# Performance work log

Measured on AMD Instinct MI355X. Metric: run time of the kernel, lower is better.

Reference implementation:

```python
import jax, jax.numpy as jnp
import numpy as np
import math

B, T, C = 32, 256, 1024
LAYER_ID, NUM_LAYERS = 12, 24
NEG_INF = -1e38


def setup_inputs() -> dict:
    key = jax.random.key(0)
    ks = jax.random.split(key, 5)
    x = jax.random.normal(ks[0], (B, T, C), dtype=jnp.float32)
    # deterministic parameter init, faithful to the torch __init__
    r01 = LAYER_ID / (NUM_LAYERS - 1)          # ratio_0_to_1
    r10 = 1.0 - LAYER_ID / NUM_LAYERS          # ratio_1_to_almost0
    h = jnp.arange(C, dtype=jnp.float32)
    time_decay = -5.0 + 8.0 * (h / (C - 1)) ** (0.7 + 1.3 * r01)
    tf = (jnp.arange(C) + 1) % 3 - 1
    time_first = jnp.full((C,), math.log(0.3), jnp.float32) + 0.5 * tf.astype(jnp.float32)
    xr = (jnp.arange(C, dtype=jnp.float32) / C)[None, None, :]   # [1,1,C]
    time_mix_k = xr ** r10
    time_mix_v = xr ** r10 + 0.3 * r01
    time_mix_r = xr ** (0.5 * r10)
    s = 1.0 / math.sqrt(C)
    Wk = jax.random.normal(ks[1], (C, C), jnp.float32) * s
    Wv = jax.random.normal(ks[2], (C, C), jnp.float32) * s
    Wr = jax.random.normal(ks[3], (C, C), jnp.float32) * s
    Wo = jax.random.normal(ks[4], (C, C), jnp.float32) * s
    return {"x": x, "time_decay": time_decay, "time_first": time_first,
            "time_mix_k": time_mix_k, "time_mix_v": time_mix_v, "time_mix_r": time_mix_r,
            "Wk": Wk, "Wv": Wv, "Wr": Wr, "Wo": Wo}


def wkv(time_decay, time_first, k, v):
    """Numerically-stabilized WKV scan. k,v: [B,T,C]; decay/first: [C]."""
    w = -jnp.exp(time_decay)   # per-channel log-decay (negative)
    u = time_first
    kT = jnp.swapaxes(k, 0, 1)  # [T,B,C]
    vT = jnp.swapaxes(v, 0, 1)

    def step(carry, kv):
        p, q, o = carry                       # p,q: running num/den; o: log scale
        kt, vt = kv                           # [B,C]
        no = jnp.maximum(o, u + kt)
        A = jnp.exp(o - no)
        Bc = jnp.exp(u + kt - no)
        y = (A * p + Bc * vt) / (A * q + Bc)
        no2 = jnp.maximum(w + o, kt)
        A2 = jnp.exp(w + o - no2)
        B2 = jnp.exp(kt - no2)
        return (A2 * p + B2 * vt, A2 * q + B2, no2), y

    init = (jnp.zeros((k.shape[0], k.shape[2]), k.dtype),
            jnp.zeros((k.shape[0], k.shape[2]), k.dtype),
            jnp.full((k.shape[0], k.shape[2]), NEG_INF, k.dtype))
    _, yT = jax.lax.scan(step, init, (kT, vT))
    return jnp.swapaxes(yT, 0, 1)  # [B,T,C]


def reference(x, time_decay, time_first, time_mix_k, time_mix_v, time_mix_r, Wk, Wv, Wr, Wo):
    # time_shift: xx[t] = x[t-1], xx[0] = 0
    xx = jnp.pad(x, ((0, 0), (1, 0), (0, 0)))[:, :-1, :]
    xk = x * time_mix_k + xx * (1.0 - time_mix_k)
    xv = x * time_mix_v + xx * (1.0 - time_mix_v)
    xr = x * time_mix_r + xx * (1.0 - time_mix_r)
    k = jnp.einsum('btc,dc->btd', xk, Wk)
    v = jnp.einsum('btc,dc->btd', xv, Wv)
    r = jnp.einsum('btc,dc->btd', xr, Wr)
    sr = jax.nn.sigmoid(r)
    rwkv = sr * wkv(time_decay, time_first, k, v)
    return jnp.einsum('btc,dc->btd', rwkv, Wo)
```

## Files before the change

### kernel.cpp

```cpp
#include <hip/hip_runtime.h>

#define Bdim 32
#define Tdim 256
#define Cdim 1024
#define Mrows (Bdim * Tdim)

typedef unsigned short u16;
typedef unsigned int u32;
typedef __bf16 bf16x8 __attribute__((ext_vector_type(8)));
typedef float f32x4 __attribute__((ext_vector_type(4)));

__device__ __forceinline__ float bf2f(u32 u) {
    union { u32 i; float f; } v; v.i = u << 16; return v.f;
}
__device__ __forceinline__ u16 f2bf(float f) {
    union { float f; u32 i; } v; v.f = f;
    u32 u = v.i;
    return (u16)((u + 0x7fffu + ((u >> 16) & 1u)) >> 16);
}

__device__ __forceinline__ void gload16(const u16* g, u16* l) {
    __builtin_amdgcn_global_load_lds(
        (__attribute__((address_space(1))) const void*)g,
        (__attribute__((address_space(3))) void*)l, 16, 0, 0);
}

__global__ __launch_bounds__(256) void prep_fused(
    const float* __restrict__ x, const float* __restrict__ tmk,
    const float* __restrict__ tmv, const float* __restrict__ tmr,
    u16* __restrict__ xk, u16* __restrict__ xv, u16* __restrict__ xr,
    const float* __restrict__ w0, const float* __restrict__ w1,
    const float* __restrict__ w2, const float* __restrict__ w3,
    u16* __restrict__ o0, u16* __restrict__ o1,
    u16* __restrict__ o2, u16* __restrict__ o3)
{
    int bid = blockIdx.x;
    if (bid < 4096) {
        int tid = bid * 256 + threadIdx.x;
        int e = tid << 3;
        int c = e & (Cdim - 1);
        int t = (e >> 10) & (Tdim - 1);
        float xf[8], xxf[8], mk[8], mv[8], mr[8];
        *(float4*)(xf)     = *(const float4*)(x + e);
        *(float4*)(xf + 4) = *(const float4*)(x + e + 4);
        if (t != 0) {
            *(float4*)(xxf)     = *(const float4*)(x + e - Cdim);
            *(float4*)(xxf + 4) = *(const float4*)(x + e - Cdim + 4);
        } else {
#pragma unroll
            for (int j = 0; j < 8; j++) xxf[j] = 0.f;
        }
        *(float4*)(mk)     = *(const float4*)(tmk + c);
        *(float4*)(mk + 4) = *(const float4*)(tmk + c + 4);
        *(float4*)(mv)     = *(const float4*)(tmv + c);
        *(float4*)(mv + 4) = *(const float4*)(tmv + c + 4);
        *(float4*)(mr)     = *(const float4*)(tmr + c);
        *(float4*)(mr + 4) = *(const float4*)(tmr + c + 4);
        u16 ok[8], ov[8], orr[8];
#pragma unroll
        for (int j = 0; j < 8; j++) {
            float d = xf[j] - xxf[j];
            ok[j]  = f2bf(xxf[j] + d * mk[j]);
            ov[j]  = f2bf(xxf[j] + d * mv[j]);
            orr[j] = f2bf(xxf[j] + d * mr[j]);
        }
        *(uint4*)(xk + e) = *(const uint4*)ok;
        *(uint4*)(xv + e) = *(const uint4*)ov;
        *(uint4*)(xr + e) = *(const uint4*)orr;
    } else {
        int wb = bid - 4096;
        int m = wb >> 9;
        const float* src; u16* dst;
        switch (m) {
            case 0: src = w0; dst = o0; break;
            case 1: src = w1; dst = o1; break;
            case 2: src = w2; dst = o2; break;
            default: src = w3; dst = o3; break;
        }
        int i = (((wb & 511) << 8) + threadIdx.x) << 3;
        float a[8];
        *(float4*)(a)     = *(const float4*)(src + i);
        *(float4*)(a + 4) = *(const float4*)(src + i + 4);
        u16 o[8];
#pragma unroll
        for (int j = 0; j < 8; j++) o[j] = f2bf(a[j]);
        *(uint4*)(dst + i) = *(const uint4*)o;
    }
}

template <int BF16OUT>
__device__ __forceinline__ void gemm_body(
    const u16* __restrict__ A, const u16* __restrict__ Bw, void* __restrict__ Cout,
    u16* As0, u16* Bs0, u16* As1, u16* Bs1, int bm, int bn)
{
    const int K = Cdim, N = Cdim;
    const int tid = threadIdx.x;
    const int lane = tid & 63, wave = tid >> 6;
    const int wm = (wave & 1) << 6, wn = (wave >> 1) << 6;
    const int fr = lane & 15, quad = lane >> 4;

    const int srow = tid >> 2;
    const int skc = ((((tid & 3) + ((tid >> 3) & 3)) & 3) << 3);
    const u16* ga = A + (size_t)(bm * 128 + srow) * K + skc;
    const u16* gb = Bw + (size_t)(bn * 128 + srow) * K + skc;
    u16* la0 = As0 + (wave << 9);
    u16* lb0 = Bs0 + (wave << 9);
    u16* la1 = As1 + (wave << 9);
    u16* lb1 = Bs1 + (wave << 9);
    const size_t gstep = (size_t)64 * K;

    f32x4 acc[4][4];
#pragma unroll
    for (int i = 0; i < 4; i++)
#pragma unroll
        for (int j = 0; j < 4; j++)
            acc[i][j] = (f32x4){0.f, 0.f, 0.f, 0.f};

    const int rq = (((quad - ((fr >> 1) & 3)) & 3) << 3);

    for (int k0 = 0; k0 < K; k0 += 64) {
        __syncthreads();
        gload16(ga, la0);
        gload16(ga + gstep, la0 + 2048);
        gload16(gb, lb0);
        gload16(gb + gstep, lb0 + 2048);
        gload16(ga + 32, la1);
        gload16(ga + 32 + gstep, la1 + 2048);
        gload16(gb + 32, lb1);
        gload16(gb + 32 + gstep, lb1 + 2048);
        ga += 64; gb += 64;
        __syncthreads();
#pragma unroll
        for (int h = 0; h < 2; h++) {
            const u16* Ah = h ? As1 : As0;
            const u16* Bh = h ? Bs1 : Bs0;
            bf16x8 af[4], bfr[4];
#pragma unroll
            for (int i = 0; i < 4; i++) {
                af[i]  = *(const bf16x8*)(Ah + (wm + i * 16 + fr) * 32 + rq);
                bfr[i] = *(const bf16x8*)(Bh + (wn + i * 16 + fr) * 32 + rq);
            }
#pragma unroll
            for (int i = 0; i < 4; i++)
#pragma unroll
                for (int j = 0; j < 4; j++)
                    acc[i][j] = __builtin_amdgcn_mfma_f32_16x16x32_bf16(
                        af[i], bfr[j], acc[i][j], 0, 0, 0);
        }
    }

    const int gr0 = bm * 128 + wm + quad * 4;
    const int gc0 = bn * 128 + wn + fr;
#pragma unroll
    for (int i = 0; i < 4; i++)
#pragma unroll
        for (int j = 0; j < 4; j++)
#pragma unroll
            for (int r = 0; r < 4; r++) {
                int gr = gr0 + i * 16 + r;
                int gc = gc0 + j * 16;
                float val = acc[i][j][r];
                if (BF16OUT)
                    ((u16*)Cout)[(size_t)gr * N + gc] = f2bf(val);
                else
                    ((float*)Cout)[(size_t)gr * N + gc] = val;
            }
}

__global__ __launch_bounds__(256) void gemm3_kernel(
    const u16* __restrict__ xk, const u16* __restrict__ xv, const u16* __restrict__ xr,
    const u16* __restrict__ wk, const u16* __restrict__ wv, const u16* __restrict__ wr,
    u16* __restrict__ ck, u16* __restrict__ cv, u16* __restrict__ cr)
{
    __shared__ u16 As0[128 * 32], Bs0[128 * 32], As1[128 * 32], Bs1[128 * 32];
    const u16* A; const u16* Bw; u16* Cout;
    switch (blockIdx.z) {
        case 0:  A = xk; Bw = wk; Cout = ck; break;
        case 1:  A = xv; Bw = wv; Cout = cv; break;
        default: A = xr; Bw = wr; Cout = cr; break;
    }
    int bx = blockIdx.x;
    gemm_body<1>(A, Bw, (void*)Cout, As0, Bs0, As1, Bs1, bx & 63, bx >> 6);
}

__global__ __launch_bounds__(256) void gemmo_kernel(
    const u16* __restrict__ A, const u16* __restrict__ Bw, float* __restrict__ Cout)
{
    __shared__ u16 As0[128 * 32], Bs0[128 * 32], As1[128 * 32], Bs1[128 * 32];
    int bx = blockIdx.x;
    gemm_body<0>(A, Bw, (void*)Cout, As0, Bs0, As1, Bs1, bx & 63, bx >> 6);
}

#define WTC 16

#define LOADCHUNK(KA, VA, RA, T0)                                        \
    _Pragma("unroll")                                                    \
    for (int s = 0; s < WTC; s++) {                                      \
        size_t idx = base + (size_t)((T0) + s) * Cdim;                   \
        KA[s] = kb[idx]; VA[s] = vb[idx]; RA[s] = rb[idx];               \
    }

#define COMPCHUNK(KA, VA, RA, T0)                                        \
    _Pragma("unroll")                                                    \
    for (int s = 0; s < WTC; s++) {                                      \
        float kt = bf2f(KA[s]);                                          \
        float vt = bf2f(VA[s]);                                          \
        float rt = bf2f(RA[s]);                                          \
        float uk = u + kt;                                               \
        float no = fmaxf(o, uk);                                         \
        float Ae = __expf(o - no);                                       \
        float Bc = __expf(uk - no);                                      \
        float num = Ae * p + Bc * vt;                                    \
        float den = Ae * q + Bc;                                         \
        float y = num * __builtin_amdgcn_rcpf(den);                      \
        float sr = __builtin_amdgcn_rcpf(1.f + __expf(-rt));             \
        rwkv[base + (size_t)((T0) + s) * Cdim] = f2bf(y * sr);           \
        float wo = w + o;                                                \
        float no2 = fmaxf(wo, kt);                                       \
        float A2 = __expf(wo - no2);                                     \
        float B2 = __expf(kt - no2);                                     \
        p = A2 * p + B2 * vt;                                            \
        q = A2 * q + B2;                                                 \
        o = no2;                                                         \
    }

__global__ __launch_bounds__(64) void wkv_kernel(
    const u16* __restrict__ kb, const u16* __restrict__ vb,
    const u16* __restrict__ rb, const float* __restrict__ td,
    const float* __restrict__ tfirst, u16* __restrict__ rwkv)
{
    int lane = threadIdx.x;
    int blk = blockIdx.x;
    int b = blk >> 4;
    int c = ((blk & 15) << 6) + lane;
    float w = -__expf(td[c]);
    float u = tfirst[c];
    const size_t base = (size_t)b * Tdim * Cdim + c;

    u32 kA[WTC], vA[WTC], rA[WTC];
    u32 kB[WTC], vB[WTC], rB[WTC];
    float p = 0.f, q = 0.f, o = -1e38f;

    LOADCHUNK(kA, vA, rA, 0)
    for (int t0 = 0; t0 < Tdim; t0 += 2 * WTC) {
        LOADCHUNK(kB, vB, rB, t0 + WTC)
        COMPCHUNK(kA, vA, rA, t0)
        if (t0 + 2 * WTC < Tdim) {
            LOADCHUNK(kA, vA, rA, t0 + 2 * WTC)
        }
        COMPCHUNK(kB, vB, rB, t0 + WTC)
    }
}

extern "C" void kernel_launch(void* const* d_in, const int* in_sizes, int n_in,
                              void* d_out, int out_size, void* d_ws, size_t ws_size,
                              hipStream_t stream) {
    (void)in_sizes; (void)n_in; (void)out_size; (void)ws_size;
    const float* x   = (const float*)d_in[0];
    const float* td  = (const float*)d_in[1];
    const float* tfi = (const float*)d_in[2];
    const float* tmk = (const float*)d_in[3];
    const float* tmv = (const float*)d_in[4];
    const float* tmr = (const float*)d_in[5];
    const float* Wk  = (const float*)d_in[6];
    const float* Wv  = (const float*)d_in[7];
    const float* Wr  = (const float*)d_in[8];
    const float* Wo  = (const float*)d_in[9];

    char* ws = (char*)d_ws;
    const size_t MiB = (size_t)1 << 20;
    u16* xk    = (u16*)(ws);
    u16* xv    = (u16*)(ws + 16 * MiB);
    u16* xr    = (u16*)(ws + 32 * MiB);
    u16* wkb   = (u16*)(ws + 48 * MiB);
    u16* wvb   = (u16*)(ws + 50 * MiB);
    u16* wrb   = (u16*)(ws + 52 * MiB);
    u16* wob   = (u16*)(ws + 54 * MiB);
    u16* kb    = (u16*)(ws + 56 * MiB);
    u16* vb    = (u16*)(ws + 72 * MiB);
    u16* rb    = (u16*)(ws + 88 * MiB);
    u16* rwkvb = (u16*)(ws);

    prep_fused<<<6144, 256, 0, stream>>>(x, tmk, tmv, tmr, xk, xv, xr,
                                         Wk, Wv, Wr, Wo, wkb, wvb, wrb, wob);

    gemm3_kernel<<<dim3(512, 1, 3), 256, 0, stream>>>(xk, xv, xr, wkb, wvb, wrb,
                                                      kb, vb, rb);

    wkv_kernel<<<512, 64, 0, stream>>>(kb, vb, rb, td, tfi, rwkvb);

    gemmo_kernel<<<512, 256, 0, stream>>>(rwkvb, wob, (float*)d_out);
}
```

Before: 227.4 us.

## Use 256x128 GEMM tiles with 8 waves and triple-buffered async LDS pipeline

```diff
diff --git a/kernel.cpp b/kernel.cpp
--- a/kernel.cpp
+++ b/kernel.cpp
@@ -3,7 +3,6 @@
 #define Bdim 32
 #define Tdim 256
 #define Cdim 1024
-#define Mrows (Bdim * Tdim)
 
 typedef unsigned short u16;
 typedef unsigned int u32;
@@ -89,25 +88,27 @@
 }
 
 template <int BF16OUT>
-__device__ __forceinline__ void gemm_body(
+__device__ __forceinline__ void gemm_body256(
     const u16* __restrict__ A, const u16* __restrict__ Bw, void* __restrict__ Cout,
-    u16* As0, u16* Bs0, u16* As1, u16* Bs1, int bm, int bn)
+    u16* As, u16* Bs, int bm, int bn)
 {
     const int K = Cdim, N = Cdim;
+    const int NT = K / 64;
     const int tid = threadIdx.x;
     const int lane = tid & 63, wave = tid >> 6;
-    const int wm = (wave & 1) << 6, wn = (wave >> 1) << 6;
+    const int wm = (wave >> 1) << 6;
+    const int wn = (wave & 1) << 6;
     const int fr = lane & 15, quad = lane >> 4;
-
-    const int srow = tid >> 2;
-    const int skc = ((((tid & 3) + ((tid >> 3) & 3)) & 3) << 3);
-    const u16* ga = A + (size_t)(bm * 128 + srow) * K + skc;
-    const u16* gb = Bw + (size_t)(bn * 128 + srow) * K + skc;
-    u16* la0 = As0 + (wave << 9);
-    u16* lb0 = Bs0 + (wave << 9);
-    u16* la1 = As1 + (wave << 9);
-    u16* lb1 = Bs1 + (wave << 9);
-    const size_t gstep = (size_t)64 * K;
+    const int lwo = wave << 9;
+
+    const int srow = tid >> 3;
+    const int schunk = ((tid & 7) ^ (srow & 7)) << 3;
+    const u16* gaS = A  + (size_t)(bm * 256 + srow) * K + schunk;
+    const u16* gbS = Bw + (size_t)(bn * 128 + srow) * K + schunk;
+    const size_t rstep = (size_t)64 * K;
+
+    const int koff0 = ((quad << 3))      ^ ((fr & 7) << 3);
+    const int koff1 = (32 + (quad << 3)) ^ ((fr & 7) << 3);
 
     f32x4 acc[4][4];
 #pragma unroll
@@ -116,40 +117,80 @@
         for (int j = 0; j < 4; j++)
             acc[i][j] = (f32x4){0.f, 0.f, 0.f, 0.f};
 
-    const int rq = (((quad - ((fr >> 1) & 3)) & 3) << 3);
-
-    for (int k0 = 0; k0 < K; k0 += 64) {
-        __syncthreads();
-        gload16(ga, la0);
-        gload16(ga + gstep, la0 + 2048);
-        gload16(gb, lb0);
-        gload16(gb + gstep, lb0 + 2048);
-        gload16(ga + 32, la1);
-        gload16(ga + 32 + gstep, la1 + 2048);
-        gload16(gb + 32, lb1);
-        gload16(gb + 32 + gstep, lb1 + 2048);
-        ga += 64; gb += 64;
-        __syncthreads();
-#pragma unroll
-        for (int h = 0; h < 2; h++) {
-            const u16* Ah = h ? As1 : As0;
-            const u16* Bh = h ? Bs1 : Bs0;
-            bf16x8 af[4], bfr[4];
-#pragma unroll
-            for (int i = 0; i < 4; i++) {
-                af[i]  = *(const bf16x8*)(Ah + (wm + i * 16 + fr) * 32 + rq);
-                bfr[i] = *(const bf16x8*)(Bh + (wn + i * 16 + fr) * 32 + rq);
+    auto issue2 = [&](int T, int aoff, int boff) {
+        const u16* ga = gaS + T * 64;
+        u16* la = As + aoff + lwo;
+        gload16(ga,             la);
+        gload16(ga + rstep,     la + 4096);
+        gload16(ga + 2 * rstep, la + 8192);
+        gload16(ga + 3 * rstep, la + 12288);
+        const u16* gb = gbS + T * 64;
+        u16* lb = Bs + boff + lwo;
+        gload16(gb,         lb);
+        gload16(gb + rstep, lb + 4096);
+    };
+
+    auto compute_tile = [&](int ac, int bc) {
+        const u16* __restrict__ Ab = As + ac;
+        const u16* __restrict__ Bb = Bs + bc;
+        __builtin_amdgcn_s_setprio(1);
+#pragma unroll
+        for (int ph = 0; ph < 4; ++ph) {
+            const int qi = ph >> 1, qj = ph & 1;
+            bf16x8 af[2][2], bfr[2][2];
+#pragma unroll
+            for (int d = 0; d < 2; ++d) {
+                const int ra = (wm + (qi * 2 + d) * 16 + fr) << 6;
+                af[d][0] = *(const bf16x8*)(Ab + ra + koff0);
+                af[d][1] = *(const bf16x8*)(Ab + ra + koff1);
+                const int rb = (wn + (qj * 2 + d) * 16 + fr) << 6;
+                bfr[d][0] = *(const bf16x8*)(Bb + rb + koff0);
+                bfr[d][1] = *(const bf16x8*)(Bb + rb + koff1);
             }
 #pragma unroll
-            for (int i = 0; i < 4; i++)
-#pragma unroll
-                for (int j = 0; j < 4; j++)
-                    acc[i][j] = __builtin_amdgcn_mfma_f32_16x16x32_bf16(
-                        af[i], bfr[j], acc[i][j], 0, 0, 0);
-        }
-    }
-
-    const int gr0 = bm * 128 + wm + quad * 4;
+            for (int di = 0; di < 2; ++di)
+#pragma unroll
+                for (int dj = 0; dj < 2; ++dj) {
+                    acc[qi * 2 + di][qj * 2 + dj] =
+                        __builtin_amdgcn_mfma_f32_16x16x32_bf16(
+                            af[di][0], bfr[dj][0], acc[qi * 2 + di][qj * 2 + dj], 0, 0, 0);
+                    acc[qi * 2 + di][qj * 2 + dj] =
+                        __builtin_amdgcn_mfma_f32_16x16x32_bf16(
+                            af[di][1], bfr[dj][1], acc[qi * 2 + di][qj * 2 + dj], 0, 0, 0);
+                }
+        }
+        __builtin_amdgcn_s_setprio(0);
+    };
+
+    issue2(0, 0, 0);
+    issue2(1, 16384, 8192);
+    asm volatile("s_waitcnt vmcnt(6)" ::: "memory");
+    __builtin_amdgcn_s_barrier();
+    __builtin_amdgcn_sched_barrier(0);
+
+    int a_c = 0, b_c = 0;
+    int a_s = 32768, b_s = 16384;
+#pragma unroll 1
+    for (int t = 0; t <= NT - 3; ++t) {
+        issue2(t + 2, a_s, b_s);
+        compute_tile(a_c, b_c);
+        asm volatile("s_waitcnt vmcnt(6)" ::: "memory");
+        __builtin_amdgcn_s_barrier();
+        __builtin_amdgcn_sched_barrier(0);
+        a_c += 16384; if (a_c == 49152) a_c = 0;
+        b_c += 8192;  if (b_c == 24576) b_c = 0;
+        a_s += 16384; if (a_s == 49152) a_s = 0;
+        b_s += 8192;  if (b_s == 24576) b_s = 0;
+    }
+    compute_tile(a_c, b_c);
+    asm volatile("s_waitcnt vmcnt(0)" ::: "memory");
+    __builtin_amdgcn_s_barrier();
+    __builtin_amdgcn_sched_barrier(0);
+    a_c += 16384; if (a_c == 49152) a_c = 0;
+    b_c += 8192;  if (b_c == 24576) b_c = 0;
+    compute_tile(a_c, b_c);
+
+    const int gr0 = bm * 256 + wm + quad * 4;
     const int gc0 = bn * 128 + wn + fr;
 #pragma unroll
     for (int i = 0; i < 4; i++)
@@ -167,12 +208,13 @@
             }
 }
 
-__global__ __launch_bounds__(256) void gemm3_kernel(
+__global__ __launch_bounds__(512) void gemm3_kernel(
     const u16* __restrict__ xk, const u16* __restrict__ xv, const u16* __restrict__ xr,
     const u16* __restrict__ wk, const u16* __restrict__ wv, const u16* __restrict__ wr,
     u16* __restrict__ ck, u16* __restrict__ cv, u16* __restrict__ cr)
 {
-    __shared__ u16 As0[128 * 32], Bs0[128 * 32], As1[128 * 32], Bs1[128 * 32];
+    __shared__ __align__(16) u16 As[3 * 16384];
+    __shared__ __align__(16) u16 Bs[3 * 8192];
     const u16* A; const u16* Bw; u16* Cout;
     switch (blockIdx.z) {
         case 0:  A = xk; Bw = wk; Cout = ck; break;
@@ -180,15 +222,16 @@
         default: A = xr; Bw = wr; Cout = cr; break;
     }
     int bx = blockIdx.x;
-    gemm_body<1>(A, Bw, (void*)Cout, As0, Bs0, As1, Bs1, bx & 63, bx >> 6);
-}
-
-__global__ __launch_bounds__(256) void gemmo_kernel(
+    gemm_body256<1>(A, Bw, (void*)Cout, As, Bs, bx & 31, bx >> 5);
+}
+
+__global__ __launch_bounds__(512) void gemmo_kernel(
     const u16* __restrict__ A, const u16* __restrict__ Bw, float* __restrict__ Cout)
 {
-    __shared__ u16 As0[128 * 32], Bs0[128 * 32], As1[128 * 32], Bs1[128 * 32];
+    __shared__ __align__(16) u16 As[3 * 16384];
+    __shared__ __align__(16) u16 Bs[3 * 8192];
     int bx = blockIdx.x;
-    gemm_body<0>(A, Bw, (void*)Cout, As0, Bs0, As1, Bs1, bx & 63, bx >> 6);
+    gemm_body256<0>(A, Bw, (void*)Cout, As, Bs, bx & 31, bx >> 5);
 }
 
 #define WTC 16
@@ -284,10 +327,10 @@
     prep_fused<<<6144, 256, 0, stream>>>(x, tmk, tmv, tmr, xk, xv, xr,
                                          Wk, Wv, Wr, Wo, wkb, wvb, wrb, wob);
 
-    gemm3_kernel<<<dim3(512, 1, 3), 256, 0, stream>>>(xk, xv, xr, wkb, wvb, wrb,
+    gemm3_kernel<<<dim3(256, 1, 3), 512, 0, stream>>>(xk, xv, xr, wkb, wvb, wrb,
                                                       kb, vb, rb);
 
     wkv_kernel<<<512, 64, 0, stream>>>(kb, vb, rb, td, tfi, rwkvb);
 
-    gemmo_kernel<<<512, 256, 0, stream>>>(rwkvb, wob, (float*)d_out);
-}
+    gemmo_kernel<<<256, 512, 0, stream>>>(rwkvb, wob, (float*)d_out);
+}
```

Result: slower. 243.7 us (+7.2%).

## Rewrite GEMMs with 256x256 tiles and phased double-buffered LDS pipeline

Applied to the files above, without the earlier changes.

```diff
diff --git a/kernel.cpp b/kernel.cpp
--- a/kernel.cpp
+++ b/kernel.cpp
@@ -3,7 +3,6 @@
 #define Bdim 32
 #define Tdim 256
 #define Cdim 1024
-#define Mrows (Bdim * Tdim)
 
 typedef unsigned short u16;
 typedef unsigned int u32;
@@ -89,70 +88,153 @@
 }
 
 template <int BF16OUT>
-__device__ __forceinline__ void gemm_body(
+__device__ __forceinline__ void gemm_body256(
     const u16* __restrict__ A, const u16* __restrict__ Bw, void* __restrict__ Cout,
-    u16* As0, u16* Bs0, u16* As1, u16* Bs1, int bm, int bn)
+    u16* __restrict__ Ls, int bm, int bn)
 {
     const int K = Cdim, N = Cdim;
+    const int NT = K / 64;
     const int tid = threadIdx.x;
     const int lane = tid & 63, wave = tid >> 6;
-    const int wm = (wave & 1) << 6, wn = (wave >> 1) << 6;
+    const int wm = wave >> 2;
+    const int wn = wave & 3;
     const int fr = lane & 15, quad = lane >> 4;
-
-    const int srow = tid >> 2;
-    const int skc = ((((tid & 3) + ((tid >> 3) & 3)) & 3) << 3);
-    const u16* ga = A + (size_t)(bm * 128 + srow) * K + skc;
-    const u16* gb = Bw + (size_t)(bn * 128 + srow) * K + skc;
-    u16* la0 = As0 + (wave << 9);
-    u16* lb0 = Bs0 + (wave << 9);
-    u16* la1 = As1 + (wave << 9);
-    u16* lb1 = Bs1 + (wave << 9);
-    const size_t gstep = (size_t)64 * K;
-
-    f32x4 acc[4][4];
-#pragma unroll
-    for (int i = 0; i < 4; i++)
+    const int fr7 = fr & 7;
+
+    const int srow = tid >> 3;
+    const int schunk = ((tid & 7) ^ (srow & 7)) << 3;
+    const u16* gA = A + (size_t)(bm * 256 + srow) * K + schunk;
+    const int gbrow = ((srow >> 5) << 6) + (srow & 31);
+    const u16* gB = Bw + (size_t)(bn * 256 + gbrow) * K + schunk;
+    u16* lA = Ls + (wave << 9);
+    u16* lB = Ls + 32768 + (wave << 9);
+
+    auto stAX = [&](int T, int buf) {
+        const u16* g = gA + T * 64;
+        u16* l = lA + buf * 16384;
+        gload16(g,                   l);
+        gload16(g + (size_t)128 * K, l + 4096);
+    };
+    auto stBX = [&](int T, int buf) {
+        const u16* g = gB + T * 64;
+        u16* l = lB + buf * 16384;
+        gload16(g,                   l);
+        gload16(g + (size_t)128 * K, l + 4096);
+    };
+    auto stBY = [&](int T, int buf) {
+        const u16* g = gB + T * 64;
+        u16* l = lB + buf * 16384;
+        gload16(g + (size_t)32 * K,  l + 8192);
+        gload16(g + (size_t)160 * K, l + 12288);
+    };
+    auto stAY = [&](int T, int buf) {
+        const u16* g = gA + T * 64;
+        u16* l = lA + buf * 16384;
+        gload16(g + (size_t)64 * K,  l + 8192);
+        gload16(g + (size_t)192 * K, l + 12288);
+    };
+
+    const int arX = wm * 64 + fr;
+    const int brX = wn * 32 + fr;
+
+    f32x4 acc[8][4];
+#pragma unroll
+    for (int i = 0; i < 8; i++)
 #pragma unroll
         for (int j = 0; j < 4; j++)
             acc[i][j] = (f32x4){0.f, 0.f, 0.f, 0.f};
 
-    const int rq = (((quad - ((fr >> 1) & 3)) & 3) << 3);
-
-    for (int k0 = 0; k0 < K; k0 += 64) {
-        __syncthreads();
-        gload16(ga, la0);
-        gload16(ga + gstep, la0 + 2048);
-        gload16(gb, lb0);
-        gload16(gb + gstep, lb0 + 2048);
-        gload16(ga + 32, la1);
-        gload16(ga + 32 + gstep, la1 + 2048);
-        gload16(gb + 32, lb1);
-        gload16(gb + 32 + gstep, lb1 + 2048);
-        ga += 64; gb += 64;
-        __syncthreads();
-#pragma unroll
-        for (int h = 0; h < 2; h++) {
-            const u16* Ah = h ? As1 : As0;
-            const u16* Bh = h ? Bs1 : Bs0;
-            bf16x8 af[4], bfr[4];
-#pragma unroll
-            for (int i = 0; i < 4; i++) {
-                af[i]  = *(const bf16x8*)(Ah + (wm + i * 16 + fr) * 32 + rq);
-                bfr[i] = *(const bf16x8*)(Bh + (wn + i * 16 + fr) * 32 + rq);
-            }
-#pragma unroll
-            for (int i = 0; i < 4; i++)
-#pragma unroll
-                for (int j = 0; j < 4; j++)
-                    acc[i][j] = __builtin_amdgcn_mfma_f32_16x16x32_bf16(
-                        af[i], bfr[j], acc[i][j], 0, 0, 0);
-        }
-    }
-
-    const int gr0 = bm * 128 + wm + quad * 4;
-    const int gc0 = bn * 128 + wn + fr;
-#pragma unroll
-    for (int i = 0; i < 4; i++)
+    bf16x8 af[4][2], b0[2][2], b1[2][2];
+
+#define KOFF(s) ((((s << 2) + quad) ^ fr7) << 3)
+#define MFMA_Q(I0, J0, BFR)                                                   \
+    _Pragma("unroll")                                                         \
+    for (int s = 0; s < 2; ++s)                                               \
+        _Pragma("unroll")                                                     \
+        for (int i = 0; i < 4; ++i)                                           \
+            _Pragma("unroll")                                                 \
+            for (int j = 0; j < 2; ++j)                                       \
+                acc[(I0) + i][(J0) + j] = __builtin_amdgcn_mfma_f32_16x16x32_bf16( \
+                    af[i][s], BFR[j][s], acc[(I0) + i][(J0) + j], 0, 0, 0);
+
+    stAX(0, 0); stBX(0, 0); stBY(0, 0); stAY(0, 0);
+    asm volatile("s_waitcnt vmcnt(4)" ::: "memory");
+    __builtin_amdgcn_s_barrier();
+
+#pragma unroll 1
+    for (int t = 0; t < NT; ++t) {
+        const int buf = t & 1, nb = buf ^ 1;
+        const u16* __restrict__ Ab = Ls + buf * 16384;
+        const u16* __restrict__ Bb = Ls + 32768 + buf * 16384;
+        const bool st = (t + 1 < NT);
+
+#pragma unroll
+        for (int i = 0; i < 4; ++i)
+#pragma unroll
+            for (int s = 0; s < 2; ++s)
+                af[i][s] = *(const bf16x8*)(Ab + (arX + i * 16) * 64 + KOFF(s));
+#pragma unroll
+        for (int j = 0; j < 2; ++j)
+#pragma unroll
+            for (int s = 0; s < 2; ++s)
+                b0[j][s] = *(const bf16x8*)(Bb + (brX + j * 16) * 64 + KOFF(s));
+        if (st) stAX(t + 1, nb);
+        __builtin_amdgcn_s_barrier();
+        asm volatile("s_waitcnt lgkmcnt(0)" ::: "memory");
+        __builtin_amdgcn_sched_barrier(0);
+        __builtin_amdgcn_s_setprio(1);
+        MFMA_Q(0, 0, b0)
+        __builtin_amdgcn_s_setprio(0);
+        if (st) { asm volatile("s_waitcnt vmcnt(4)" ::: "memory"); }
+        else    { asm volatile("s_waitcnt vmcnt(2)" ::: "memory"); }
+        __builtin_amdgcn_s_barrier();
+
+#pragma unroll
+        for (int j = 0; j < 2; ++j)
+#pragma unroll
+            for (int s = 0; s < 2; ++s)
+                b1[j][s] = *(const bf16x8*)(Bb + (128 + brX + j * 16) * 64 + KOFF(s));
+        if (st) stBX(t + 1, nb);
+        __builtin_amdgcn_s_barrier();
+        asm volatile("s_waitcnt lgkmcnt(0)" ::: "memory");
+        __builtin_amdgcn_sched_barrier(0);
+        __builtin_amdgcn_s_setprio(1);
+        MFMA_Q(0, 2, b1)
+        __builtin_amdgcn_s_setprio(0);
+        if (st) { asm volatile("s_waitcnt vmcnt(4)" ::: "memory"); }
+        else    { asm volatile("s_waitcnt vmcnt(0)" ::: "memory"); }
+        __builtin_amdgcn_s_barrier();
+
+#pragma unroll
+        for (int i = 0; i < 4; ++i)
+#pragma unroll
+            for (int s = 0; s < 2; ++s)
+                af[i][s] = *(const bf16x8*)(Ab + (128 + arX + i * 16) * 64 + KOFF(s));
+        if (st) stBY(t + 1, nb);
+        __builtin_amdgcn_s_barrier();
+        asm volatile("s_waitcnt lgkmcnt(0)" ::: "memory");
+        __builtin_amdgcn_sched_barrier(0);
+        __builtin_amdgcn_s_setprio(1);
+        MFMA_Q(4, 2, b1)
+        __builtin_amdgcn_s_setprio(0);
+        if (st) { asm volatile("s_waitcnt vmcnt(4)" ::: "memory"); }
+        __builtin_amdgcn_s_barrier();
+
+        if (st) stAY(t + 1, nb);
+        __builtin_amdgcn_s_barrier();
+        __builtin_amdgcn_s_setprio(1);
+        MFMA_Q(4, 0, b0)
+        __builtin_amdgcn_s_setprio(0);
+        if (st) { asm volatile("s_waitcnt vmcnt(4)" ::: "memory"); }
+        __builtin_amdgcn_s_barrier();
+    }
+#undef MFMA_Q
+#undef KOFF
+
+    const int gr0 = bm * 256 + wm * 128 + quad * 4;
+    const int gc0 = bn * 256 + wn * 64 + fr;
+#pragma unroll
+    for (int i = 0; i < 8; i++)
 #pragma unroll
         for (int j = 0; j < 4; j++)
 #pragma unroll
@@ -167,12 +249,12 @@
             }
 }
 
-__global__ __launch_bounds__(256) void gemm3_kernel(
+__global__ __launch_bounds__(512, 2) void gemm3_kernel(
     const u16* __restrict__ xk, const u16* __restrict__ xv, const u16* __restrict__ xr,
     const u16* __restrict__ wk, const u16* __restrict__ wv, const u16* __restrict__ wr,
     u16* __restrict__ ck, u16* __restrict__ cv, u16* __restrict__ cr)
 {
-    __shared__ u16 As0[128 * 32], Bs0[128 * 32], As1[128 * 32], Bs1[128 * 32];
+    __shared__ __align__(16) u16 Ls[4 * 16384];
     const u16* A; const u16* Bw; u16* Cout;
     switch (blockIdx.z) {
         case 0:  A = xk; Bw = wk; Cout = ck; break;
@@ -180,15 +262,15 @@
         default: A = xr; Bw = wr; Cout = cr; break;
     }
     int bx = blockIdx.x;
-    gemm_body<1>(A, Bw, (void*)Cout, As0, Bs0, As1, Bs1, bx & 63, bx >> 6);
-}
-
-__global__ __launch_bounds__(256) void gemmo_kernel(
+    gemm_body256<1>(A, Bw, (void*)Cout, Ls, bx & 31, bx >> 5);
+}
+
+__global__ __launch_bounds__(512, 2) void gemmo_kernel(
     const u16* __restrict__ A, const u16* __restrict__ Bw, float* __restrict__ Cout)
 {
-    __shared__ u16 As0[128 * 32], Bs0[128 * 32], As1[128 * 32], Bs1[128 * 32];
+    __shared__ __align__(16) u16 Ls[4 * 16384];
     int bx = blockIdx.x;
-    gemm_body<0>(A, Bw, (void*)Cout, As0, Bs0, As1, Bs1, bx & 63, bx >> 6);
+    gemm_body256<0>(A, Bw, (void*)Cout, Ls, bx & 31, bx >> 5);
 }
 
 #define WTC 16
@@ -284,10 +366,10 @@
     prep_fused<<<6144, 256, 0, stream>>>(x, tmk, tmv, tmr, xk, xv, xr,
                                          Wk, Wv, Wr, Wo, wkb, wvb, wrb, wob);
 
-    gemm3_kernel<<<dim3(512, 1, 3), 256, 0, stream>>>(xk, xv, xr, wkb, wvb, wrb,
+    gemm3_kernel<<<dim3(128, 1, 3), 512, 0, stream>>>(xk, xv, xr, wkb, wvb, wrb,
                                                       kb, vb, rb);
 
     wkv_kernel<<<512, 64, 0, stream>>>(kb, vb, rb, td, tfi, rwkvb);
 
-    gemmo_kernel<<<512, 256, 0, stream>>>(rwkvb, wob, (float*)d_out);
-}
+    gemmo_kernel<<<128, 512, 0, stream>>>(rwkvb, wob, (float*)d_out);
+}
```

Result: slower. 240.4 us (+5.7%).

## Double-buffer GEMM LDS tiles to overlap global loads with MFMA compute

Applied to the files above, without the earlier changes.

```diff
diff --git a/kernel.cpp b/kernel.cpp
--- a/kernel.cpp
+++ b/kernel.cpp
@@ -3,7 +3,6 @@
 #define Bdim 32
 #define Tdim 256
 #define Cdim 1024
-#define Mrows (Bdim * Tdim)
 
 typedef unsigned short u16;
 typedef unsigned int u32;
@@ -91,9 +90,10 @@
 template <int BF16OUT>
 __device__ __forceinline__ void gemm_body(
     const u16* __restrict__ A, const u16* __restrict__ Bw, void* __restrict__ Cout,
-    u16* As0, u16* Bs0, u16* As1, u16* Bs1, int bm, int bn)
+    u16* __restrict__ Ls, int bm, int bn)
 {
     const int K = Cdim, N = Cdim;
+    const int NT = K / 64;
     const int tid = threadIdx.x;
     const int lane = tid & 63, wave = tid >> 6;
     const int wm = (wave & 1) << 6, wn = (wave >> 1) << 6;
@@ -103,11 +103,22 @@
     const int skc = ((((tid & 3) + ((tid >> 3) & 3)) & 3) << 3);
     const u16* ga = A + (size_t)(bm * 128 + srow) * K + skc;
     const u16* gb = Bw + (size_t)(bn * 128 + srow) * K + skc;
-    u16* la0 = As0 + (wave << 9);
-    u16* lb0 = Bs0 + (wave << 9);
-    u16* la1 = As1 + (wave << 9);
-    u16* lb1 = Bs1 + (wave << 9);
     const size_t gstep = (size_t)64 * K;
+    const int lw = wave << 9;
+
+    auto stage = [&](int t, int buf) {
+        const u16* gat = ga + t * 64;
+        const u16* gbt = gb + t * 64;
+        u16* base = Ls + buf * 16384 + lw;
+        gload16(gat,              base);
+        gload16(gat + gstep,      base + 2048);
+        gload16(gbt,              base + 4096);
+        gload16(gbt + gstep,      base + 4096 + 2048);
+        gload16(gat + 32,         base + 8192);
+        gload16(gat + 32 + gstep, base + 8192 + 2048);
+        gload16(gbt + 32,         base + 12288);
+        gload16(gbt + 32 + gstep, base + 12288 + 2048);
+    };
 
     f32x4 acc[4][4];
 #pragma unroll
@@ -118,22 +129,19 @@
 
     const int rq = (((quad - ((fr >> 1) & 3)) & 3) << 3);
 
-    for (int k0 = 0; k0 < K; k0 += 64) {
-        __syncthreads();
-        gload16(ga, la0);
-        gload16(ga + gstep, la0 + 2048);
-        gload16(gb, lb0);
-        gload16(gb + gstep, lb0 + 2048);
-        gload16(ga + 32, la1);
-        gload16(ga + 32 + gstep, la1 + 2048);
-        gload16(gb + 32, lb1);
-        gload16(gb + 32 + gstep, lb1 + 2048);
-        ga += 64; gb += 64;
-        __syncthreads();
+    stage(0, 0);
+    asm volatile("s_waitcnt vmcnt(0)" ::: "memory");
+    __builtin_amdgcn_s_barrier();
+
+#pragma unroll 1
+    for (int t = 0; t < NT; ++t) {
+        const int buf = t & 1;
+        if (t + 1 < NT) stage(t + 1, buf ^ 1);
+        const u16* __restrict__ Tb = Ls + buf * 16384;
 #pragma unroll
         for (int h = 0; h < 2; h++) {
-            const u16* Ah = h ? As1 : As0;
-            const u16* Bh = h ? Bs1 : Bs0;
+            const u16* Ah = Tb + h * 8192;
+            const u16* Bh = Tb + 4096 + h * 8192;
             bf16x8 af[4], bfr[4];
 #pragma unroll
             for (int i = 0; i < 4; i++) {
@@ -147,6 +155,8 @@
                     acc[i][j] = __builtin_amdgcn_mfma_f32_16x16x32_bf16(
                         af[i], bfr[j], acc[i][j], 0, 0, 0);
         }
+        asm volatile("s_waitcnt vmcnt(0) lgkmcnt(0)" ::: "memory");
+        __builtin_amdgcn_s_barrier();
     }
 
     const int gr0 = bm * 128 + wm + quad * 4;
@@ -172,7 +182,7 @@
     const u16* __restrict__ wk, const u16* __restrict__ wv, const u16* __restrict__ wr,
     u16* __restrict__ ck, u16* __restrict__ cv, u16* __restrict__ cr)
 {
-    __shared__ u16 As0[128 * 32], Bs0[128 * 32], As1[128 * 32], Bs1[128 * 32];
+    __shared__ __align__(16) u16 Ls[2 * 16384];
     const u16* A; const u16* Bw; u16* Cout;
     switch (blockIdx.z) {
         case 0:  A = xk; Bw = wk; Cout = ck; break;
@@ -180,15 +190,15 @@
         default: A = xr; Bw = wr; Cout = cr; break;
     }
     int bx = blockIdx.x;
-    gemm_body<1>(A, Bw, (void*)Cout, As0, Bs0, As1, Bs1, bx & 63, bx >> 6);
+    gemm_body<1>(A, Bw, (void*)Cout, Ls, bx & 63, bx >> 6);
 }
 
 __global__ __launch_bounds__(256) void gemmo_kernel(
     const u16* __restrict__ A, const u16* __restrict__ Bw, float* __restrict__ Cout)
 {
-    __shared__ u16 As0[128 * 32], Bs0[128 * 32], As1[128 * 32], Bs1[128 * 32];
+    __shared__ __align__(16) u16 Ls[2 * 16384];
     int bx = blockIdx.x;
-    gemm_body<0>(A, Bw, (void*)Cout, As0, Bs0, As1, Bs1, bx & 63, bx >> 6);
+    gemm_body<0>(A, Bw, (void*)Cout, Ls, bx & 63, bx >> 6);
 }
 
 #define WTC 16
```

Result: no change. 226.9 us (-0.2%).
